# Kernel tuning notes

Hardware: AMD Instinct MI355X
Metric: run time of the kernel (lower is better)

Reference implementation:

```python
import jax, jax.numpy as jnp
from jax import lax
import numpy as np

# Constants from CVLNet utils (get_meter_per_pixel() and SatMap_original_sidelength)
METER_PER_PIXEL = 0.2
SATMAP_ORIGINAL_SIDELENGTH = 512.0
SHIFT_RANGE = 32
EPS = 1e-12


def _l2_normalize_per_sample(x):
    # F.normalize(x.reshape(B, -1)) : L2-normalize each sample over all elements
    B = x.shape[0]
    norm = jnp.linalg.norm(x.reshape(B, -1), axis=1)
    norm = jnp.maximum(norm, EPS).reshape((B,) + (1,) * (x.ndim - 1))
    return x / norm


def setup_inputs() -> dict:
    key = jax.random.key(0)
    k1, k2 = jax.random.split(key)
    grd_feature = jax.random.normal(k1, (4, 32, 64, 64), dtype=jnp.float32)   # (N,C,Hk,Wk)
    sat_feature = jax.random.normal(k2, (32, 32, 64, 64), dtype=jnp.float32)  # (M,C,Hs,Ws)
    return {"grd_feature": grd_feature, "sat_feature": sat_feature, "uncertainty": 1}


def reference(grd_feature, sat_feature, uncertainty):
    N, C, H_k, W_k = grd_feature.shape
    grd = _l2_normalize_per_sample(grd_feature)

    s = SHIFT_RANGE
    sat = jnp.pad(sat_feature, ((0, 0), (0, 0), (s, s), (s, s)))
    M, _, H_i, W_i = sat.shape
    sat = _l2_normalize_per_sample(sat)  # zero-padding does not change the norm

    # F.conv2d(sat.repeat(1,N,1,1), grd, groups=N) == plain cross-correlation of
    # every sat map with every grd template: output [M, N, Ho, Wo]
    corr = lax.conv_general_dilated(
        sat, grd, window_strides=(1, 1), padding='VALID',
        dimension_numbers=('NCHW', 'OIHW', 'NCHW'))

    # avg_pool2d(sat^2, (Hk,Wk), stride=1, divisor_override=1) summed over C ==
    # sliding-window sum of per-pixel squared norms
    s2 = jnp.sum(sat * sat, axis=1, keepdims=True)  # [M,1,Hi,Wi]
    partical = lax.reduce_window(s2, 0.0, lax.add,
                                 window_dimensions=(1, 1, H_k, W_k),
                                 window_strides=(1, 1, 1, 1), padding='VALID')
    denom = jnp.maximum(jnp.sqrt(partical) * uncertainty, EPS)
    corr = corr / denom

    similarity_matrix = jnp.max(corr, axis=(2, 3))  # [M,N]

    Wo = corr.shape[-1]
    max_index = jnp.argmax(corr.reshape(M, N, -1), axis=-1)
    row = (max_index // Wo).astype(jnp.float32)
    col = (max_index % Wo).astype(jnp.float32)
    half = Wo / 2.0
    max_pos = jnp.stack([-(row - half), col - half], axis=-1)  # [M,N,2]
    shift_meters = max_pos * METER_PER_PIXEL * SATMAP_ORIGINAL_SIDELENGTH / W_i
    return (similarity_matrix, shift_meters)
```

## Files before the change

### kernel.cpp

```cpp
#include <hip/hip_runtime.h>
#include <math.h>

#define N_GRD 4
#define M_SAT 32
#define C_CH  32
#define HK    64
#define WK    64
#define HO    65
#define WO    65
#define SAMPLE_ELEMS (C_CH * HK * WK)

typedef _Float16 h8 __attribute__((ext_vector_type(8)));
typedef float    f4 __attribute__((ext_vector_type(4)));
typedef unsigned int u32;

#define OFF_INV    0
#define OFF_S      64
#define OFF_CANDV  135264
#define OFF_CANDI  135776
#define OFF_DOTS   136288
#define OFF_PART   136800
#define OFF_G2F    956000
#define OFF_SH     1824352
#define G2_HALFS   1736704

#define G2_BLOCKS  6784
#define SH_BLOCKS  2048
#define PREP_BLOCKS (G2_BLOCKS + SH_BLOCKS + M_SAT + N_GRD)

__global__ __launch_bounds__(256) void prep_kernel(const float* __restrict__ grd,
                                                   const float* __restrict__ sat,
                                                   _Float16* __restrict__ g2,
                                                   _Float16* __restrict__ sh,
                                                   float* __restrict__ S,
                                                   float* __restrict__ inv) {
    const int bx = blockIdx.x;
    const int tid = threadIdx.x;
    __shared__ float s2[64][65];

    if (bx < G2_BLOCKS) {
        int idx = bx * 256 + tid;
        int c = idx & 3; int t = idx >> 2;
        int js = t % 106; t /= 106;
        int n = t & 3; t >>= 2;
        int i = t & 63; t >>= 6;
        int cq = t & 7; int cp = t >> 3;
        int j = js - 16 - cp;
        float v = 0.0f;
        if (j >= 0 && j < 64)
            v = grd[(((size_t)n * 32 + (cq * 4 + c)) * 64 + i) * 64 + j];
        g2[idx] = (_Float16)v;
        return;
    }
    if (bx < G2_BLOCKS + SH_BLOCKS) {
        int idx = (bx - G2_BLOCKS) * 256 + tid;
        int gr = idx & 31;
        int r  = (idx >> 5) & 63;
        int cq = (idx >> 11) & 7;
        int mm = idx >> 14;
        const float* sp = sat + (((size_t)mm * 32 + cq * 4) * 64 + r) * 64 + gr * 2;
        float2 v0 = *(const float2*)(sp);
        float2 v1 = *(const float2*)(sp + 4096);
        float2 v2 = *(const float2*)(sp + 8192);
        float2 v3 = *(const float2*)(sp + 12288);
        h8 hv = {(_Float16)v0.x, (_Float16)v1.x, (_Float16)v2.x, (_Float16)v3.x,
                 (_Float16)v0.y, (_Float16)v1.y, (_Float16)v2.y, (_Float16)v3.y};
        *(h8*)(sh + (size_t)idx * 8) = hv;
        return;
    }
    if (bx < G2_BLOCKS + SH_BLOCKS + M_SAT) {
        const int m = bx - G2_BLOCKS - SH_BLOCKS;
        const float* base = sat + (size_t)m * SAMPLE_ELEMS;
        for (int p = tid; p < HK * WK; p += 256) {
            float s = 0.0f;
            for (int c = 0; c < C_CH; ++c) {
                float v = base[c * (HK * WK) + p];
                s += v * v;
            }
            s2[p >> 6][p & 63] = s;
        }
        __syncthreads();
        if (tid < 64) {
            int r = tid; float run = 0.0f;
            for (int w = 0; w < 64; ++w) { run += s2[r][w]; s2[r][w] = run; }
        }
        __syncthreads();
        if (tid < 64) {
            int c = tid; float run = 0.0f;
            for (int h = 0; h < 64; ++h) { run += s2[h][c]; s2[h][c] = run; }
        }
        __syncthreads();
        if (tid == 0)
            inv[N_GRD + m] = 1.0f / fmaxf(sqrtf(s2[63][63]), 1e-12f);
        float* Sm = S + (size_t)m * (HO * WO);
        for (int p = tid; p < HO * WO; p += 256) {
            int r = p / 65, c = p - r * 65;
            Sm[p] = (r == 0 || c == 0) ? 0.0f : s2[r - 1][c - 1];
        }
        return;
    }
    {
        const int b = bx - G2_BLOCKS - SH_BLOCKS - M_SAT;
        const float4* v = reinterpret_cast<const float4*>(grd + (size_t)b * SAMPLE_ELEMS);
        float ss = 0.0f;
        for (int p = tid; p < SAMPLE_ELEMS / 4; p += 256) {
            float4 q = v[p];
            ss += q.x * q.x + q.y * q.y + q.z * q.z + q.w * q.w;
        }
        for (int off = 32; off > 0; off >>= 1) ss += __shfl_down(ss, off);
        __shared__ float ls[4];
        int lane = tid & 63, w = tid >> 6;
        if (lane == 0) ls[w] = ss;
        __syncthreads();
        if (tid == 0)
            inv[b] = 1.0f / fmaxf(sqrtf(ls[0] + ls[1] + ls[2] + ls[3]), 1e-12f);
    }
}

__global__ __launch_bounds__(256, 2) void corr_mfma_kernel(const _Float16* __restrict__ sh,
                                                           const _Float16* __restrict__ g2,
                                                           float* __restrict__ partial) {
    __shared__ __align__(16) char lds[75520];
    char* AB = lds;
    char* BB = lds + 48384;

    const int m  = blockIdx.x;
    const int xs = blockIdx.y;
    const int z  = blockIdx.z;
    const int h  = z & 1;
    const int qt = z >> 1;

    const int x00 = (xs < 4) ? 16 * xs : 49;
    const int qb  = (xs < 4) ? 16 * xs : 48;
    const int xoff = x00 - qb;
    const int qstage = qb + 40 * h;

    const int tid  = threadIdx.x;
    const int w    = tid >> 6;
    const int lane = tid & 63;
    const int s    = lane & 15;
    const int u    = lane >> 4;
    const int cp   = (s + xoff) & 1;

    f4 acc[5][4];
#pragma unroll
    for (int t = 0; t < 5; ++t)
#pragma unroll
        for (int n = 0; n < 4; ++n) { acc[t][n][0]=0.f; acc[t][n][1]=0.f; acc[t][n][2]=0.f; acc[t][n][3]=0.f; }

    const int bbase = ((w * 2 + cp) * 4 * 106 + (16 + cp + 40 * h + 2 * u - s - xoff)) * 8;
    const int abase0 = s * 336 + u * 16;
    const int q2base = qstage >> 1;

    for (int cqi = 0; cqi < 2; ++cqi) {
        const int cq = qt * 2 + cqi;
        __syncthreads();
        for (int k = 0; k < 11; ++k) {
            int idx = k * 256 + tid;
            if (idx < 2688) {
                u32 r = (u32)idx / 21u;
                u32 g = (u32)idx - r * 21u;
                int q2 = q2base + (int)g;
                bool valid = (g < 20u) & (r >= 32u) & (r < 96u) & (q2 >= 16) & (q2 < 48);
                const _Float16* src = valid
                    ? sh + ((((size_t)m * 8 + cq) * 64 + (r - 32)) * 32 + (q2 - 16)) * 8
                    : g2;
                __builtin_amdgcn_global_load_lds(
                    (const __attribute__((address_space(1))) u32*)(const void*)src,
                    (__attribute__((address_space(3))) u32*)(void*)(AB + k * 4096 + w * 1024),
                    16, 0, 0);
            }
        }
        for (int ii = 0; ii < 16; ++ii) {
            __syncthreads();
            for (int k = 0; k < 7; ++k) {
                int idx = k * 256 + tid;
                if (idx < 1696) {
                    int wi = idx / 424;  int rm  = idx - wi * 424;
                    int cpp = rm / 212;  int rm2 = rm - cpp * 212;
                    int nn = rm2 / 53;   int jg  = rm2 - nn * 53;
                    int iw = wi * 16 + ii;
                    const _Float16* gsrc = g2 + (size_t)((((cpp * 8 + cq) * 64 + iw) * 4 + nn)) * 424 + jg * 8;
                    __builtin_amdgcn_global_load_lds(
                        (const __attribute__((address_space(1))) u32*)(const void*)gsrc,
                        (__attribute__((address_space(3))) u32*)(void*)(BB + k * 4096 + w * 1024),
                        16, 0, 0);
                }
            }
            __syncthreads();
            const char* Ab = AB + abase0 + (w * 16 + ii) * 336;
            const char* Bb = BB + bbase;
#pragma unroll
            for (int qs = 0; qs < 5; ++qs) {
                h8 a[5]; h8 bfr[4];
#pragma unroll
                for (int n = 0; n < 4; ++n) bfr[n] = *(const h8*)(Bb + qs * 64 + n * 848);
#pragma unroll
                for (int t = 0; t < 5; ++t) a[t] = *(const h8*)(Ab + qs * 64 + t * 5376);
#pragma unroll
                for (int t = 0; t < 5; ++t)
#pragma unroll
                    for (int n = 0; n < 4; ++n)
                        acc[t][n] = __builtin_amdgcn_mfma_f32_16x16x32_f16(a[t], bfr[n], acc[t][n], 0, 0, 0);
            }
        }
    }

    float* red = (float*)lds;
#pragma unroll
    for (int t = 0; t < 5; ++t) {
        __syncthreads();
#pragma unroll
        for (int nn = 0; nn < 4; ++nn)
            *(f4*)(red + ((nn * 4 + w) * 64 + lane) * 4) = acc[t][nn];
        __syncthreads();
        {
            int nn = tid >> 6, ln = tid & 63;
            f4 sum = *(f4*)(red + ((nn * 4 + 0) * 64 + ln) * 4);
            sum = sum + *(f4*)(red + ((nn * 4 + 1) * 64 + ln) * 4);
            sum = sum + *(f4*)(red + ((nn * 4 + 2) * 64 + ln) * 4);
            sum = sum + *(f4*)(red + ((nn * 4 + 3) * 64 + ln) * 4);
            int ss = ln & 15, uu = ln >> 4;
            float* dst = partial + ((size_t)(m * 4 + nn)) * 6400
                         + (xs * 16 + ss) * 80 + t * 16 + uu * 4;
#pragma unroll
            for (int l = 0; l < 4; ++l) atomicAdd(dst + l, sum[l]);
        }
    }
}

__global__ __launch_bounds__(256) void epilogue_kernel(const float* __restrict__ partial,
                                                       const float* __restrict__ S,
                                                       const float* __restrict__ inv,
                                                       const int* __restrict__ unc,
                                                       float* __restrict__ candv,
                                                       int* __restrict__ candi) {
    const int b = blockIdx.x;
    const int m = b >> 2, n = b & 3;
    const int tid = threadIdx.x;
    const float uu = (float)unc[0];
    const float sc = inv[n] * inv[N_GRD + m];
    const float isn = inv[N_GRD + m];
    const float* Sm = S + (size_t)m * 4225;
    const float* pb = partial + (size_t)(m * 4 + n) * 6400;

    float best = -3.4e38f;
    int bidx = 0x7fffffff;
    for (int pp = tid; pp < 4225; pp += 256) {
        int x = pp / 65, y = pp - x * 65;
        int xsl = (x == 64) ? 79 : x;
        float raw = pb[xsl * 80 + y];
        float num = raw * sc;
        int r0 = max(0, y - 32), r1 = min(64, y + 32);
        int q0 = max(0, x - 32), q1 = min(64, x + 32);
        float ps = Sm[r1 * 65 + q1] - Sm[r0 * 65 + q1] - Sm[r1 * 65 + q0] + Sm[r0 * 65 + q0];
        float denom = fmaxf(sqrtf(ps) * isn * uu, 1e-12f);
        float v = num / denom;
        int p = y * 65 + x;
        if (v > best || (v == best && p < bidx)) { best = v; bidx = p; }
    }
    __shared__ float bv[256]; __shared__ int bi[256];
    __shared__ float cv[256]; __shared__ int ci[256];
    __shared__ int winner;
    bv[tid] = best; bi[tid] = bidx;
    __syncthreads();
    for (int round = 0; round < 4; ++round) {
        cv[tid] = bv[tid]; ci[tid] = bi[tid];
        __syncthreads();
        for (int st = 128; st > 0; st >>= 1) {
            if (tid < st) {
                float ov = cv[tid + st]; int oi = ci[tid + st];
                if (ov > cv[tid] || (ov == cv[tid] && oi < ci[tid])) { cv[tid] = ov; ci[tid] = oi; }
            }
            __syncthreads();
        }
        if (tid == 0) { candv[b * 4 + round] = cv[0]; candi[b * 4 + round] = ci[0]; winner = ci[0]; }
        __syncthreads();
        if (bi[tid] == winner) bv[tid] = -3.4e38f;
        __syncthreads();
    }
}

__global__ __launch_bounds__(256) void refine_dot_kernel(const float* __restrict__ grd,
                                                         const float* __restrict__ sat,
                                                         const float* __restrict__ candv,
                                                         const int* __restrict__ candi,
                                                         float* __restrict__ dots) {
    const int b = blockIdx.x;
    const int k = blockIdx.y;
    const int cq = blockIdx.z;
    const int m = b >> 2, n = b & 3;
    float v0 = candv[b * 4];
    float thr = v0 - (0.02f * fabsf(v0) + 1e-4f);
    if (k > 0 && candv[b * 4 + k] < thr) return;
    int p = candi[b * 4 + k];
    int y = p / 65, x = p - y * 65;
    const int tid = threadIdx.x, lane = tid & 63, w = tid >> 6;
    const int ilo = max(0, 32 - y), ihi = min(64, 96 - y);
    int xj = x + lane - 32;
    float acc = 0.0f;
    if (xj >= 0 && xj < 64) {
        const float* sm = sat + (size_t)m * SAMPLE_ELEMS;
        const float* gn = grd + (size_t)n * SAMPLE_ELEMS;
        for (int cc = 0; cc < 4; ++cc) {
            const int cbase = (cq * 4 + cc) << 12;
            const float* sp = sm + cbase + xj + ((y - 32) << 6);
            const float* gp = gn + cbase + lane;
            for (int i = ilo + w; i < ihi; i += 4)
                acc = fmaf(sp[i << 6], gp[i << 6], acc);
        }
    }
    for (int off = 32; off > 0; off >>= 1) acc += __shfl_down(acc, off);
    __shared__ float ls[4];
    if (lane == 0) ls[w] = acc;
    __syncthreads();
    if (tid == 0) atomicAdd(&dots[b * 4 + k], ls[0] + ls[1] + ls[2] + ls[3]);
}

__global__ __launch_bounds__(128) void refine_pick_kernel(const float* __restrict__ S,
                                                          const float* __restrict__ inv,
                                                          const int* __restrict__ unc,
                                                          const float* __restrict__ candv,
                                                          const int* __restrict__ candi,
                                                          const float* __restrict__ dots,
                                                          float* __restrict__ out) {
    int b = threadIdx.x;
    if (b >= 128) return;
    const int m = b >> 2, n = b & 3;
    const float uu = (float)unc[0];
    const float sc = inv[n] * inv[N_GRD + m];
    const float isn = inv[N_GRD + m];
    const float* Sm = S + (size_t)m * 4225;
    float v0 = candv[b * 4];
    float thr = v0 - (0.02f * fabsf(v0) + 1e-4f);
    float bestv = -3.4e38f; int bestp = 0x7fffffff;
    for (int k = 0; k < 4; ++k) {
        if (k > 0 && candv[b * 4 + k] < thr) break;
        int p = candi[b * 4 + k];
        int y = p / 65, x = p - y * 65;
        int r0 = max(0, y - 32), r1 = min(64, y + 32);
        int q0 = max(0, x - 32), q1 = min(64, x + 32);
        float ps = Sm[r1 * 65 + q1] - Sm[r0 * 65 + q1] - Sm[r1 * 65 + q0] + Sm[r0 * 65 + q0];
        float denom = fmaxf(sqrtf(ps) * isn * uu, 1e-12f);
        float v = dots[b * 4 + k] * sc / denom;
        if (v > bestv || (v == bestv && p < bestp)) { bestv = v; bestp = p; }
    }
    out[b] = bestv;
    int row = bestp / 65, col = bestp - row * 65;
    float pr = -((float)row - 32.5f);
    float pc = (float)col - 32.5f;
    out[128 + b * 2 + 0] = ((pr * 0.2f) * 512.0f) * (1.0f / 128.0f);
    out[128 + b * 2 + 1] = ((pc * 0.2f) * 512.0f) * (1.0f / 128.0f);
}

extern "C" void kernel_launch(void* const* d_in, const int* in_sizes, int n_in,
                              void* d_out, int out_size, void* d_ws, size_t ws_size,
                              hipStream_t stream) {
    const float* grd = (const float*)d_in[0];
    const float* sat = (const float*)d_in[1];
    const int*   unc = (const int*)d_in[2];
    float* out = (float*)d_out;
    float* ws  = (float*)d_ws;

    float* inv     = ws + OFF_INV;
    float* S       = ws + OFF_S;
    float* candv   = ws + OFF_CANDV;
    int*   candi   = (int*)(ws + OFF_CANDI);
    float* dots    = ws + OFF_DOTS;
    float* partial = ws + OFF_PART;
    _Float16* g2   = (_Float16*)(ws + OFF_G2F);
    _Float16* sh   = (_Float16*)(ws + OFF_SH);

    hipMemsetAsync(partial, 0, 819200 * sizeof(float), stream);
    hipMemsetAsync(dots, 0, 512 * sizeof(float), stream);
    prep_kernel<<<PREP_BLOCKS, 256, 0, stream>>>(grd, sat, g2, sh, S, inv);
    corr_mfma_kernel<<<dim3(M_SAT, 5, 8), 256, 0, stream>>>(sh, g2, partial);
    epilogue_kernel<<<M_SAT * N_GRD, 256, 0, stream>>>(partial, S, inv, unc, candv, candi);
    refine_dot_kernel<<<dim3(128, 4, 8), 256, 0, stream>>>(grd, sat, candv, candi, dots);
    refine_pick_kernel<<<1, 128, 0, stream>>>(S, inv, unc, candv, candi, dots, out);
}
```

Before: 375.7 us.

## Pre-swizzle grd into MFMA fragment layout, read B directly from global

```diff
diff --git a/kernel.cpp b/kernel.cpp
--- a/kernel.cpp
+++ b/kernel.cpp
@@ -20,56 +20,44 @@
 #define OFF_CANDI  135776
 #define OFF_DOTS   136288
 #define OFF_PART   136800
-#define OFF_G2F    956000
-#define OFF_SH     1824352
-#define G2_HALFS   1736704
-
-#define G2_BLOCKS  6784
-#define SH_BLOCKS  2048
-#define PREP_BLOCKS (G2_BLOCKS + SH_BLOCKS + M_SAT + N_GRD)
+#define OFF_FRAG   956000
+#define FRAG_GRANULES 1572864
+#define FRAG_BLOCKS   6144
+#define PREP_BLOCKS (FRAG_BLOCKS + M_SAT + N_GRD)
 
 __global__ __launch_bounds__(256) void prep_kernel(const float* __restrict__ grd,
                                                    const float* __restrict__ sat,
-                                                   _Float16* __restrict__ g2,
-                                                   _Float16* __restrict__ sh,
+                                                   _Float16* __restrict__ frag,
                                                    float* __restrict__ S,
                                                    float* __restrict__ inv) {
     const int bx = blockIdx.x;
     const int tid = threadIdx.x;
     __shared__ float s2[64][65];
 
-    if (bx < G2_BLOCKS) {
+    if (bx < FRAG_BLOCKS) {
         int idx = bx * 256 + tid;
-        int c = idx & 3; int t = idx >> 2;
-        int js = t % 106; t /= 106;
+        int lane = idx & 63; int t = idx >> 6;
         int n = t & 3; t >>= 2;
         int i = t & 63; t >>= 6;
-        int cq = t & 7; int cp = t >> 3;
-        int j = js - 16 - cp;
-        float v = 0.0f;
-        if (j >= 0 && j < 64)
-            v = grd[(((size_t)n * 32 + (cq * 4 + c)) * 64 + i) * 64 + j];
-        g2[idx] = (_Float16)v;
+        int cq = t & 7; int jg = t >> 3;
+        int s = lane & 15, u = lane >> 4;
+        int jb = jg * 8 - 16 + 2 * u - s;
+        const float* gb = grd + ((size_t)n * 32 + cq * 4) * 4096 + i * 64;
+        h8 hv = {0, 0, 0, 0, 0, 0, 0, 0};
+#pragma unroll
+        for (int q2 = 0; q2 < 2; ++q2) {
+            int j = jb + q2;
+            if (j >= 0 && j < 64) {
+#pragma unroll
+                for (int c = 0; c < 4; ++c)
+                    hv[q2 * 4 + c] = (_Float16)gb[c * 4096 + j];
+            }
+        }
+        *(h8*)(frag + (size_t)idx * 8) = hv;
         return;
     }
-    if (bx < G2_BLOCKS + SH_BLOCKS) {
-        int idx = (bx - G2_BLOCKS) * 256 + tid;
-        int gr = idx & 31;
-        int r  = (idx >> 5) & 63;
-        int cq = (idx >> 11) & 7;
-        int mm = idx >> 14;
-        const float* sp = sat + (((size_t)mm * 32 + cq * 4) * 64 + r) * 64 + gr * 2;
-        float2 v0 = *(const float2*)(sp);
-        float2 v1 = *(const float2*)(sp + 4096);
-        float2 v2 = *(const float2*)(sp + 8192);
-        float2 v3 = *(const float2*)(sp + 12288);
-        h8 hv = {(_Float16)v0.x, (_Float16)v1.x, (_Float16)v2.x, (_Float16)v3.x,
-                 (_Float16)v0.y, (_Float16)v1.y, (_Float16)v2.y, (_Float16)v3.y};
-        *(h8*)(sh + (size_t)idx * 8) = hv;
-        return;
-    }
-    if (bx < G2_BLOCKS + SH_BLOCKS + M_SAT) {
-        const int m = bx - G2_BLOCKS - SH_BLOCKS;
+    if (bx < FRAG_BLOCKS + M_SAT) {
+        const int m = bx - FRAG_BLOCKS;
         const float* base = sat + (size_t)m * SAMPLE_ELEMS;
         for (int p = tid; p < HK * WK; p += 256) {
             float s = 0.0f;
@@ -100,7 +88,7 @@
         return;
     }
     {
-        const int b = bx - G2_BLOCKS - SH_BLOCKS - M_SAT;
+        const int b = bx - FRAG_BLOCKS - M_SAT;
         const float4* v = reinterpret_cast<const float4*>(grd + (size_t)b * SAMPLE_ELEMS);
         float ss = 0.0f;
         for (int p = tid; p < SAMPLE_ELEMS / 4; p += 256) {
@@ -117,12 +105,10 @@
     }
 }
 
-__global__ __launch_bounds__(256, 2) void corr_mfma_kernel(const _Float16* __restrict__ sh,
-                                                           const _Float16* __restrict__ g2,
+__global__ __launch_bounds__(256, 3) void corr_mfma_kernel(const float* __restrict__ sat,
+                                                           const _Float16* __restrict__ frag,
                                                            float* __restrict__ partial) {
-    __shared__ __align__(16) char lds[75520];
-    char* AB = lds;
-    char* BB = lds + 48384;
+    __shared__ __align__(16) char AB[48384];
 
     const int m  = blockIdx.x;
     const int xs = blockIdx.y;
@@ -130,17 +116,15 @@
     const int h  = z & 1;
     const int qt = z >> 1;
 
-    const int x00 = (xs < 4) ? 16 * xs : 49;
-    const int qb  = (xs < 4) ? 16 * xs : 48;
-    const int xoff = x00 - qb;
+    const int qb     = (xs < 4) ? 16 * xs : 48;
     const int qstage = qb + 40 * h;
+    const int qoff   = 5 * h + ((xs < 4) ? 2 : 0);
 
     const int tid  = threadIdx.x;
     const int w    = tid >> 6;
     const int lane = tid & 63;
     const int s    = lane & 15;
     const int u    = lane >> 4;
-    const int cp   = (s + xoff) & 1;
 
     f4 acc[5][4];
 #pragma unroll
@@ -148,9 +132,8 @@
 #pragma unroll
         for (int n = 0; n < 4; ++n) { acc[t][n][0]=0.f; acc[t][n][1]=0.f; acc[t][n][2]=0.f; acc[t][n][3]=0.f; }
 
-    const int bbase = ((w * 2 + cp) * 4 * 106 + (16 + cp + 40 * h + 2 * u - s - xoff)) * 8;
     const int abase0 = s * 336 + u * 16;
-    const int q2base = qstage >> 1;
+    const char* fragB = (const char*)frag;
 
     for (int cqi = 0; cqi < 2; ++cqi) {
         const int cq = qt * 2 + cqi;
@@ -158,43 +141,33 @@
         for (int k = 0; k < 11; ++k) {
             int idx = k * 256 + tid;
             if (idx < 2688) {
-                u32 r = (u32)idx / 21u;
-                u32 g = (u32)idx - r * 21u;
-                int q2 = q2base + (int)g;
-                bool valid = (g < 20u) & (r >= 32u) & (r < 96u) & (q2 >= 16) & (q2 < 48);
-                const _Float16* src = valid
-                    ? sh + ((((size_t)m * 8 + cq) * 64 + (r - 32)) * 32 + (q2 - 16)) * 8
-                    : g2;
-                __builtin_amdgcn_global_load_lds(
-                    (const __attribute__((address_space(1))) u32*)(const void*)src,
-                    (__attribute__((address_space(3))) u32*)(void*)(AB + k * 4096 + w * 1024),
-                    16, 0, 0);
-            }
-        }
+                int r = idx / 21;
+                int g = idx - r * 21;
+                int q = qstage + 2 * g;
+                h8 hv = {0, 0, 0, 0, 0, 0, 0, 0};
+                if (g < 20 && r >= 32 && r < 96 && q >= 32 && q < 96) {
+                    const float* sp = sat + (((size_t)(m * 32 + cq * 4)) * 64 + (r - 32)) * 64 + (q - 32);
+                    float2 v0 = *(const float2*)(sp);
+                    float2 v1 = *(const float2*)(sp + 4096);
+                    float2 v2 = *(const float2*)(sp + 8192);
+                    float2 v3 = *(const float2*)(sp + 12288);
+                    hv[0] = (_Float16)v0.x; hv[1] = (_Float16)v1.x; hv[2] = (_Float16)v2.x; hv[3] = (_Float16)v3.x;
+                    hv[4] = (_Float16)v0.y; hv[5] = (_Float16)v1.y; hv[6] = (_Float16)v2.y; hv[7] = (_Float16)v3.y;
+                }
+                *(h8*)(AB + idx * 16) = hv;
+            }
+        }
+        __syncthreads();
+        const char* bq0 = fragB + ((size_t)(qoff * 8 + cq) * 64 + w * 16) * 4096 + lane * 16;
         for (int ii = 0; ii < 16; ++ii) {
-            __syncthreads();
-            for (int k = 0; k < 7; ++k) {
-                int idx = k * 256 + tid;
-                if (idx < 1696) {
-                    int wi = idx / 424;  int rm  = idx - wi * 424;
-                    int cpp = rm / 212;  int rm2 = rm - cpp * 212;
-                    int nn = rm2 / 53;   int jg  = rm2 - nn * 53;
-                    int iw = wi * 16 + ii;
-                    const _Float16* gsrc = g2 + (size_t)((((cpp * 8 + cq) * 64 + iw) * 4 + nn)) * 424 + jg * 8;
-                    __builtin_amdgcn_global_load_lds(
-                        (const __attribute__((address_space(1))) u32*)(const void*)gsrc,
-                        (__attribute__((address_space(3))) u32*)(void*)(BB + k * 4096 + w * 1024),
-                        16, 0, 0);
-                }
-            }
-            __syncthreads();
             const char* Ab = AB + abase0 + (w * 16 + ii) * 336;
-            const char* Bb = BB + bbase;
+            const char* Bq = bq0 + ii * 4096;
 #pragma unroll
             for (int qs = 0; qs < 5; ++qs) {
                 h8 a[5]; h8 bfr[4];
 #pragma unroll
-                for (int n = 0; n < 4; ++n) bfr[n] = *(const h8*)(Bb + qs * 64 + n * 848);
+                for (int n = 0; n < 4; ++n)
+                    bfr[n] = *(const h8*)(Bq + (size_t)qs * 2097152 + n * 1024);
 #pragma unroll
                 for (int t = 0; t < 5; ++t) a[t] = *(const h8*)(Ab + qs * 64 + t * 5376);
 #pragma unroll
@@ -206,7 +179,7 @@
         }
     }
 
-    float* red = (float*)lds;
+    float* red = (float*)AB;
 #pragma unroll
     for (int t = 0; t < 5; ++t) {
         __syncthreads();
@@ -248,8 +221,7 @@
     int bidx = 0x7fffffff;
     for (int pp = tid; pp < 4225; pp += 256) {
         int x = pp / 65, y = pp - x * 65;
-        int xsl = (x == 64) ? 79 : x;
-        float raw = pb[xsl * 80 + y];
+        float raw = pb[x * 80 + y];
         float num = raw * sc;
         int r0 = max(0, y - 32), r1 = min(64, y + 32);
         int q0 = max(0, x - 32), q1 = min(64, x + 32);
@@ -368,13 +340,12 @@
     int*   candi   = (int*)(ws + OFF_CANDI);
     float* dots    = ws + OFF_DOTS;
     float* partial = ws + OFF_PART;
-    _Float16* g2   = (_Float16*)(ws + OFF_G2F);
-    _Float16* sh   = (_Float16*)(ws + OFF_SH);
+    _Float16* frag = (_Float16*)(ws + OFF_FRAG);
 
     hipMemsetAsync(partial, 0, 819200 * sizeof(float), stream);
     hipMemsetAsync(dots, 0, 512 * sizeof(float), stream);
-    prep_kernel<<<PREP_BLOCKS, 256, 0, stream>>>(grd, sat, g2, sh, S, inv);
-    corr_mfma_kernel<<<dim3(M_SAT, 5, 8), 256, 0, stream>>>(sh, g2, partial);
+    prep_kernel<<<PREP_BLOCKS, 256, 0, stream>>>(grd, sat, frag, S, inv);
+    corr_mfma_kernel<<<dim3(M_SAT, 5, 8), 256, 0, stream>>>(sat, frag, partial);
     epilogue_kernel<<<M_SAT * N_GRD, 256, 0, stream>>>(partial, S, inv, unc, candv, candi);
     refine_dot_kernel<<<dim3(128, 4, 8), 256, 0, stream>>>(grd, sat, candv, candi, dots);
     refine_pick_kernel<<<1, 128, 0, stream>>>(S, inv, unc, candv, candi, dots, out);
```

Result: slower. 408.2 us (+8.6%).
